# Optimization experiments

Hardware: AMD Instinct MI355X
Metric: run time of the kernel (lower is better)

The kernel has to match this reference:

```python
import jax, jax.numpy as jnp
import numpy as np

N, D = 131072, 128
NUM_BOOK, K = 4, 1024


def setup_inputs() -> dict:
    key = jax.random.key(0)
    k1, k2 = jax.random.split(key)
    x = jax.random.normal(k1, (N, D), dtype=jnp.float32)
    codebooks = jax.random.normal(k2, (NUM_BOOK, K, D), dtype=jnp.float32)
    return {"x": x, "codebooks": codebooks}


def reference(x, codebooks):
    # Original: for each book i, idx = argmin_k cdist(x, C_i, p=2); stack -> [N, num_book].
    # argmin over Euclidean distance == argmin over squared distance, so we use
    # affect argmin). All num_book lookups batched in one einsum.
    dots = jnp.einsum('nd,bkd->bnk', x, codebooks)          # [B, N, K]
    c_sq = jnp.sum(codebooks * codebooks, axis=-1)          # [B, K]
    sq_dist = c_sq[:, None, :] - 2.0 * dots                 # [B, N, K]
    idx = jnp.argmin(sq_dist, axis=-1)                      # [B, N]
    return jnp.transpose(idx, (1, 0))                       # [N, num_book], int
```

## Files before the change

### kernel.cpp

```cpp
#include <hip/hip_runtime.h>
#include <math.h>

#define N_PTS  131072
#define DIM    128
#define NBOOK  4
#define KCODES 1024

#define CHUNK   32
#define NCHB    32
#define PT      2
#define BPTS    256
#define SLOTS   9
#define CHUNK_BYTES (SLOTS * 1024)
#define CHUNK_U16   (SLOTS * 512)
#define EPS_ACC 0.05f
#define WLB_CAP 32768

typedef _Float16 f16x8 __attribute__((ext_vector_type(8)));
typedef float    f32x16 __attribute__((ext_vector_type(16)));
typedef unsigned short u16;
typedef unsigned long long u64;

#define WS_RES_OFF  1179648u
#define WS_CSQ_OFF  2359296u
#define WS_CNT_OFF  (WS_CSQ_OFF + 16384u)
#define WS_WL_OFF   (WS_CNT_OFF + 256u)

__device__ inline u16 f16bits(_Float16 h) {
    union { _Float16 f; u16 u; } c; c.f = h; return c.u;
}

__device__ inline void async_copy16(const void* g, void* l) {
    __builtin_amdgcn_global_load_lds(
        (const __attribute__((address_space(1))) void*)g,
        (__attribute__((address_space(3))) void*)l,
        16, 0, 0);
}

__global__ __launch_bounds__(256)
void prep_kernel(const float* __restrict__ cb, char* __restrict__ cbf,
                 float* __restrict__ csq, int* __restrict__ counters) {
    if (blockIdx.x >= 256) {
        int idx = (blockIdx.x - 256) * 256 + threadIdx.x;
        if (idx < 4) counters[idx] = 0;
        const float4* p = (const float4*)(cb + (size_t)idx * DIM);
        float s = 0.f;
#pragma unroll
        for (int i = 0; i < DIM / 4; ++i) {
            float4 v = p[i];
            s += v.x * v.x + v.y * v.y + v.z * v.z + v.w * v.w;
        }
        csq[idx] = s;
        int b = idx >> 10, k = idx & 1023;
        _Float16 hi  = (_Float16)s;
        float    r1  = s - (float)hi;
        _Float16 mid = (_Float16)r1;
        _Float16 rem = (_Float16)(r1 - (float)mid);
        u16* dst = (u16*)(cbf + (size_t)(b * 32 + (k >> 5)) * CHUNK_BYTES
                              + 8192 + (size_t)(k & 31) * 16);
        u16 o[8] = {f16bits(hi), f16bits(mid), f16bits(rem), (u16)0x5D00, 0, 0, 0, 0};
#pragma unroll
        for (int j = 0; j < 8; ++j) dst[j] = o[j];
        u16* dz = dst + 32 * 8;
#pragma unroll
        for (int j = 0; j < 8; ++j) dz[j] = 0;
        return;
    }
    int t    = blockIdx.x * 256 + threadIdx.x;
    int lane = t & 63;
    int s    = (t >> 6) & 7;
    int bc   = t >> 9;
    int code = (bc & 31) * CHUNK + (lane & 31);
    int b    = bc >> 5;
    int dd   = s * 16 + (lane >> 5) * 8;

    const float* row = cb + ((size_t)b * KCODES + code) * DIM + dd;
    float4 v0 = ((const float4*)row)[0];
    float4 v1 = ((const float4*)row)[1];
    float vals[8] = {v0.x, v0.y, v0.z, v0.w, v1.x, v1.y, v1.z, v1.w};
    u16 o[8];
#pragma unroll
    for (int j = 0; j < 8; ++j) o[j] = f16bits((_Float16)vals[j]);
    u16* dst = (u16*)(cbf + (size_t)bc * CHUNK_BYTES + (size_t)s * 1024 + (size_t)lane * 16);
#pragma unroll
    for (int j = 0; j < 8; ++j) dst[j] = o[j];
}

__global__ __launch_bounds__(256, 3)
void argmin_mfma_kernel(const float* __restrict__ x,
                        const u16*  __restrict__ cbf,
                        int* __restrict__ out,
                        int* __restrict__ counters,
                        int* __restrict__ worklist,
                        u64* __restrict__ results) {
    __shared__ u16 lds[2 * CHUNK_U16];

    const int tid  = threadIdx.x;
    const int lane = tid & 63;
    const int w    = tid >> 6;
    const int n0   = blockIdx.x * BPTS;
    const int col  = lane & 31;
    const int kh   = lane >> 5;

    const char* src0 = (const char*)cbf + (size_t)(blockIdx.y * 64) * CHUNK_BYTES;

    auto issue = [&](int c) {
        const char* src = src0 + (size_t)c * CHUNK_BYTES;
        char* dst = (char*)&lds[(c & 1) * CHUNK_U16];
#pragma unroll
        for (int i = 0; i < 2; ++i)
            async_copy16(src + i * 4096 + tid * 16, dst + i * 4096 + w * 1024);
        if (w == 0)
            async_copy16(src + 8192 + lane * 16, dst + 8192);
    };

    issue(0);

    f16x8 xh[PT][8];
#pragma unroll
    for (int pt = 0; pt < PT; ++pt) {
        const float* xrow = x + (size_t)(n0 + w * 64 + pt * 32 + col) * DIM;
#pragma unroll
        for (int s = 0; s < 8; ++s) {
            const float* p = xrow + s * 16 + kh * 8;
            float4 v0 = *(const float4*)p;
            float4 v1 = *(const float4*)(p + 4);
            float vals[8] = {v0.x, v0.y, v0.z, v0.w, v1.x, v1.y, v1.z, v1.w};
            f16x8 hv;
#pragma unroll
            for (int j = 0; j < 8; ++j) hv[j] = (_Float16)vals[j];
            xh[pt][s] = hv;
        }
    }
    f16x8 xcf;
#pragma unroll
    for (int j = 0; j < 8; ++j) {
        _Float16 v = (_Float16)0.0f;
        if (kh == 0) {
            if (j < 3) v = (_Float16)(-0.5f);
            else if (j == 3) v = (_Float16)1.0f;
        }
        xcf[j] = v;
    }

    unsigned b1p[PT], b2p[PT];
    int bchunk[PT];
#pragma unroll
    for (int pt = 0; pt < PT; ++pt) { b1p[pt] = 0u; b2p[pt] = 0u; bchunk[pt] = 0; }

    auto mfma_chunk = [&](const u16* A, f32x16* ac) {
#pragma unroll
        for (int pt = 0; pt < PT; ++pt)
#pragma unroll
            for (int r = 0; r < 16; ++r) ac[pt][r] = 0.f;
#pragma unroll
        for (int s = 0; s < 8; ++s) {
            f16x8 ah = *(const f16x8*)&A[s * 512 + lane * 8];
#pragma unroll
            for (int pt = 0; pt < PT; ++pt)
                ac[pt] = __builtin_amdgcn_mfma_f32_32x32x16_f16(ah, xh[pt][s], ac[pt], 0, 0, 0);
        }
        f16x8 acs = *(const f16x8*)&A[8 * 512 + lane * 8];
#pragma unroll
        for (int pt = 0; pt < PT; ++pt)
            ac[pt] = __builtin_amdgcn_mfma_f32_32x32x16_f16(acs, xcf, ac[pt], 0, 0, 0);
    };

    auto epilogue = [&](const f32x16* ac, int cc) {
        int ci = cc & 31;
#pragma unroll
        for (int pt = 0; pt < PT; ++pt) {
            unsigned prev = b1p[pt], p1v = prev, p2v = b2p[pt];
#pragma unroll
            for (int r = 0; r < 16; r += 2) {
                unsigned pa = (__float_as_uint(ac[pt][r])     & 0xFFFFFFE0u) | (31u - (unsigned)r);
                unsigned pb = (__float_as_uint(ac[pt][r + 1]) & 0xFFFFFFE0u) | (30u - (unsigned)r);
                unsigned hi = pa > pb ? pa : pb;
                unsigned lo = pa < pb ? pa : pb;
                unsigned t2 = hi < p1v ? hi : p1v;
                unsigned m  = lo > t2 ? lo : t2;
                p2v = p2v > m ? p2v : m;
                p1v = p1v > hi ? p1v : hi;
            }
            bchunk[pt] = (p1v != prev) ? ci : bchunk[pt];
            b1p[pt] = p1v; b2p[pt] = p2v;
        }
    };

    auto finalize = [&](int book) {
        int b = blockIdx.y * 2 + book;
#pragma unroll
        for (int pt = 0; pt < PT; ++pt) {
            unsigned r = 31u - (b1p[pt] & 31u);
            float m1 = __uint_as_float(b1p[pt] & 0xFFFFFFE0u);
            float m2 = __uint_as_float(b2p[pt] & 0xFFFFFFE0u);
            int row = (int)((r & 3u) + 8u * (r >> 2)) + 4 * kh;
            int code = bchunk[pt] * CHUNK + row;
            float om1 = __shfl_xor(m1, 32);
            float om2 = __shfl_xor(m2, 32);
            int   oc  = __shfl_xor(code, 32);
            bool take = (om1 > m1) || (om1 == m1 && oc < code);
            float nm2 = fmaxf(fminf(m1, om1), fmaxf(m2, om2));
            if (take) { m1 = om1; code = oc; }
            m2 = nm2;
            if (lane < 32) {
                int point = n0 + w * 64 + pt * 32 + col;
                out[point * NBOOK + b] = code;
                if (m1 - m2 < EPS_ACC) {
                    int pos = atomicAdd(&counters[b], 1);
                    if (pos < WLB_CAP) {
                        worklist[b * WLB_CAP + pos] = point;
                        results[b * WLB_CAP + pos] = 0xFFFFFFFFFFFFFFFFull;
                    }
                }
            }
            b1p[pt] = 0u; b2p[pt] = 0u; bchunk[pt] = 0;
        }
    };

    __syncthreads();

    f32x16 acc0[PT], acc1[PT];
    for (int c = 0; c < 64; c += 2) {
        issue(c + 1);
        mfma_chunk(lds, acc0);
        if (c > 0) {
            epilogue(acc1, c - 1);
            if (c == 32) finalize(0);
        }
        __syncthreads();

        if (c + 2 < 64) issue(c + 2);
        mfma_chunk(lds + CHUNK_U16, acc1);
        epilogue(acc0, c);
        __syncthreads();
    }
    epilogue(acc1, 63);
    finalize(1);
}

__global__ __launch_bounds__(256)
void exact_kernel(const float* __restrict__ x,
                  const float* __restrict__ cb,
                  const float* __restrict__ csq,
                  const int* __restrict__ counters,
                  const int* __restrict__ worklist,
                  u64* __restrict__ results) {
    const int b = blockIdx.y;
    int n = counters[b];
    if (n > WLB_CAP) n = WLB_CAP;
    const int lane = threadIdx.x & 63;
    const int w    = threadIdx.x >> 6;
    const int g    = lane >> 4;
    const int d0   = (lane & 15) * 8;
    const float* cbb = cb + (size_t)b * KCODES * DIM;
    const float* csb = csq + b * KCODES;

    int units = n * 8;
    for (int u = blockIdx.x * 4 + w; u < units; u += gridDim.x * 4) {
        int i = u >> 3, q = u & 7;
        int point = worklist[b * WLB_CAP + i];
        const float* xr = x + (size_t)point * DIM + d0;
        float4 xa = ((const float4*)xr)[0];
        float4 xb = ((const float4*)xr)[1];
        float bd = 3.4e38f;
        int   bi = 0;
        int   c00 = q * 128;
#pragma unroll 4
        for (int it = 0; it < 32; ++it) {
            int c = c00 + it * 4 + g;
            const float* cr = cbb + (size_t)c * DIM + d0;
            float4 ca = ((const float4*)cr)[0];
            float4 cc = ((const float4*)cr)[1];
            float p = xa.x * ca.x + xa.y * ca.y + xa.z * ca.z + xa.w * ca.w
                    + xb.x * cc.x + xb.y * cc.y + xb.z * cc.z + xb.w * cc.w;
            p += __shfl_xor(p, 1);
            p += __shfl_xor(p, 2);
            p += __shfl_xor(p, 4);
            p += __shfl_xor(p, 8);
            float dist = csb[c] - 2.f * p;
            if (dist < bd) { bd = dist; bi = c; }
        }
#pragma unroll
        for (int off = 16; off <= 32; off <<= 1) {
            float od = __shfl_xor(bd, off);
            int   oi = __shfl_xor(bi, off);
            if (od < bd || (od == bd && oi < bi)) { bd = od; bi = oi; }
        }
        if (lane == 0) {
            unsigned ub = __float_as_uint(bd);
            ub = (ub & 0x80000000u) ? ~ub : (ub | 0x80000000u);
            u64 key = ((u64)ub << 32) | (unsigned)bi;
            atomicMin(&results[b * WLB_CAP + i], key);
        }
    }
}

__global__ __launch_bounds__(256)
void write_kernel(const int* __restrict__ counters,
                  const int* __restrict__ worklist,
                  const u64* __restrict__ results,
                  int* __restrict__ out) {
    const int b = blockIdx.y;
    int n = counters[b];
    if (n > WLB_CAP) n = WLB_CAP;
    for (int i = blockIdx.x * 256 + threadIdx.x; i < n; i += gridDim.x * 256) {
        int point = worklist[b * WLB_CAP + i];
        out[point * NBOOK + b] = (int)(results[b * WLB_CAP + i] & 1023u);
    }
}

extern "C" void kernel_launch(void* const* d_in, const int* in_sizes, int n_in,
                              void* d_out, int out_size, void* d_ws, size_t ws_size,
                              hipStream_t stream) {
    const float* x  = (const float*)d_in[0];
    const float* cb = (const float*)d_in[1];
    int* out = (int*)d_out;

    char* ws = (char*)d_ws;
    u16*   cbf      = (u16*)ws;
    u64*   results  = (u64*)(ws + WS_RES_OFF);
    float* csq      = (float*)(ws + WS_CSQ_OFF);
    int*   counters = (int*)(ws + WS_CNT_OFF);
    int*   worklist = (int*)(ws + WS_WL_OFF);

    prep_kernel<<<272, 256, 0, stream>>>(cb, (char*)cbf, csq, counters);

    argmin_mfma_kernel<<<dim3(N_PTS / BPTS, 2), 256, 0, stream>>>(x, cbf, out, counters,
                                                                  worklist, results);

    exact_kernel<<<dim3(512, 4), 256, 0, stream>>>(x, cb, csq, counters, worklist, results);

    write_kernel<<<dim3(32, 4), 256, 0, stream>>>(counters, worklist, results, out);
}
```

Before: 380.4 us.

## Remap exact rescoring to one point per lane with register-held query rows

The exact fp32 rescoring kernel used to give each wave one point, with the 128 dimensions split across lanes and a shuffle reduction per code. It now gives each lane its own worklist point, keeps that point's full 128-float row in registers, and loops over 128 codes. Every lane in the wave reads the same codebook row, so those loads are broadcast, and both the shuffle reductions and the cross-lane argmin merge go away. The cost is heavy register use (128 floats per lane), which can lower occupancy. Tail lanes are clamped to index 0 and issue a redundant atomicMin for that entry.

```diff
diff --git a/kernel.cpp b/kernel.cpp
--- a/kernel.cpp
+++ b/kernel.cpp
@@ -249,50 +249,47 @@
     const int b = blockIdx.y;
     int n = counters[b];
     if (n > WLB_CAP) n = WLB_CAP;
+    if (n == 0) return;
     const int lane = threadIdx.x & 63;
     const int w    = threadIdx.x >> 6;
-    const int g    = lane >> 4;
-    const int d0   = (lane & 15) * 8;
     const float* cbb = cb + (size_t)b * KCODES * DIM;
     const float* csb = csq + b * KCODES;
 
-    int units = n * 8;
+    int ntiles = (n + 63) >> 6;
+    int units  = ntiles * 8;
     for (int u = blockIdx.x * 4 + w; u < units; u += gridDim.x * 4) {
-        int i = u >> 3, q = u & 7;
-        int point = worklist[b * WLB_CAP + i];
-        const float* xr = x + (size_t)point * DIM + d0;
-        float4 xa = ((const float4*)xr)[0];
-        float4 xb = ((const float4*)xr)[1];
+        int tile = u >> 3, q = u & 7;
+        int ii = tile * 64 + lane;
+        int iw = ii < n ? ii : 0;
+        int point = worklist[b * WLB_CAP + iw];
+
+        const float4* xr4 = (const float4*)(x + (size_t)point * DIM);
+        float4 xr[32];
+#pragma unroll
+        for (int j = 0; j < 32; ++j) xr[j] = xr4[j];
+
         float bd = 3.4e38f;
         int   bi = 0;
-        int   c00 = q * 128;
-#pragma unroll 4
-        for (int it = 0; it < 32; ++it) {
-            int c = c00 + it * 4 + g;
-            const float* cr = cbb + (size_t)c * DIM + d0;
-            float4 ca = ((const float4*)cr)[0];
-            float4 cc = ((const float4*)cr)[1];
-            float p = xa.x * ca.x + xa.y * ca.y + xa.z * ca.z + xa.w * ca.w
-                    + xb.x * cc.x + xb.y * cc.y + xb.z * cc.z + xb.w * cc.w;
-            p += __shfl_xor(p, 1);
-            p += __shfl_xor(p, 2);
-            p += __shfl_xor(p, 4);
-            p += __shfl_xor(p, 8);
-            float dist = csb[c] - 2.f * p;
+        int   c0 = q * 128;
+        for (int cc = 0; cc < 128; ++cc) {
+            int c = c0 + cc;
+            const float4* cr = (const float4*)(cbb + (size_t)c * DIM);
+            float ax = 0.f, ay = 0.f, az = 0.f, aw = 0.f;
+#pragma unroll
+            for (int j = 0; j < 32; ++j) {
+                float4 cv = cr[j];
+                ax = fmaf(cv.x, xr[j].x, ax);
+                ay = fmaf(cv.y, xr[j].y, ay);
+                az = fmaf(cv.z, xr[j].z, az);
+                aw = fmaf(cv.w, xr[j].w, aw);
+            }
+            float dist = csb[c] - 2.f * ((ax + ay) + (az + aw));
             if (dist < bd) { bd = dist; bi = c; }
         }
-#pragma unroll
-        for (int off = 16; off <= 32; off <<= 1) {
-            float od = __shfl_xor(bd, off);
-            int   oi = __shfl_xor(bi, off);
-            if (od < bd || (od == bd && oi < bi)) { bd = od; bi = oi; }
-        }
-        if (lane == 0) {
-            unsigned ub = __float_as_uint(bd);
-            ub = (ub & 0x80000000u) ? ~ub : (ub | 0x80000000u);
-            u64 key = ((u64)ub << 32) | (unsigned)bi;
-            atomicMin(&results[b * WLB_CAP + i], key);
-        }
+        unsigned ub = __float_as_uint(bd);
+        ub = (ub & 0x80000000u) ? ~ub : (ub | 0x80000000u);
+        u64 key = ((u64)ub << 32) | (unsigned)bi;
+        atomicMin(&results[b * WLB_CAP + iw], key);
     }
 }
 
```

Measured after the change: 466.9 us. 1.23x slower.
